# Performance work log

Measured on AMD Instinct MI355X. Metric: run time of the kernel, lower is better.

## Reference

```python
import jax, jax.numpy as jnp
import numpy as np

HEIGHT = 32
SIGMA = 2.0
NUM_NEGATIVE = 4096
N, C = 32, 512
L = HEIGHT * HEIGHT


def _grid_weight(height: int, sigma: float) -> jnp.ndarray:
    # distance_weights: pairwise Euclidean distance between grid points
    ii, jj = np.meshgrid(np.arange(height), np.arange(height), indexing='ij')
    coords = np.stack([ii.ravel(), jj.ravel()], axis=1).astype(np.float32)  # [L, 2]
    d2 = ((coords[:, None, :] - coords[None, :, :]) ** 2).sum(-1)  # squared dist [L, L]
    w = -(0.5 / sigma ** 2) * d2
    np.fill_diagonal(w, -np.inf)
    return jax.nn.softmax(jnp.asarray(w, dtype=jnp.float32), axis=1)


def setup_inputs() -> dict:
    key = jax.random.key(0)
    k1, k2 = jax.random.split(key)
    embedding = jax.random.normal(k1, (N, L, C), dtype=jnp.float32)
    weight = _grid_weight(HEIGHT, SIGMA)  # [L, L] softmax-normalized grid kernel
    neg_indices = jax.random.randint(k2, (NUM_NEGATIVE,), 0, N * L, dtype=jnp.int64)
    return {"embedding": embedding, "weight": weight, "neg_indices": neg_indices}


def reference(embedding, weight, neg_indices):
    n, l, c = embedding.shape
    # F.normalize(dim=-1), eps=1e-12
    norm = jnp.maximum(jnp.linalg.norm(embedding, axis=-1, keepdims=True), 1e-12)
    e = embedding / norm  # [N, L, C]
    # target = weight @ e  (broadcast over batch)
    target = jnp.einsum('kl,nlc->nkc', weight, e)  # [N, L, C]
    sim_pos = jnp.sum(e * target, axis=-1)  # [N, L]
    flat = e.reshape(-1, c)  # [N*L, C]
    negatives = flat[neg_indices]  # [M, C]
    sim_neg = jnp.einsum('nlc,mc->nlm', e, negatives)  # [N, L, M]
    logits = jnp.concatenate([sim_pos[..., None], sim_neg], axis=2).reshape(n * l, 1 + neg_indices.shape[0])
    # CrossEntropyLoss with target class 0, mean reduction
    loss = -jnp.mean(jax.nn.log_softmax(logits, axis=-1)[:, 0])
    return loss
```

## Files before the change

kernel.cpp:

```cpp
#include <hip/hip_runtime.h>
#include <hip/hip_bf16.h>
#include <stdint.h>

#define L_DIM 1024
#define C_DIM 512
#define CB4 256
#define N_BATCH 32
#define M_NEG 4096
#define NROWS (N_BATCH * L_DIM)

typedef float f32x4 __attribute__((ext_vector_type(4)));
typedef int i32x4 __attribute__((ext_vector_type(4)));
typedef int i32x8 __attribute__((ext_vector_type(8)));

#define E4_SCALE 32.0f
#define MX_SCALE 122
#define FMT_FP4 4

template <int GOFF>
__device__ __forceinline__ void gl_lds16(const uint8_t* g, uint8_t* l) {
  __builtin_amdgcn_global_load_lds(
      (const __attribute__((address_space(1))) void*)g,
      (__attribute__((address_space(3))) void*)l, 16, GOFF, 0);
}

__device__ __forceinline__ uint32_t fp4_enc(float x) {
  const uint32_t s = (__float_as_uint(x) >> 31) << 3;
  const float a = fabsf(x);
  uint32_t c;
  c = a < 0.25f ? 0u
    : a < 0.75f ? 1u
    : a < 1.25f ? 2u
    : a < 1.75f ? 3u
    : a < 2.5f  ? 4u
    : a < 3.5f  ? 5u
    : a < 5.0f  ? 6u : 7u;
  return s | c;
}

__device__ __forceinline__ i32x8 fp4_op(i32x4 d) {
  return __builtin_shufflevector(d, d, 0, 1, 2, 3, -1, -1, -1, -1);
}

__device__ __forceinline__ int swz(int row) { return (row >> 1) & 3; }

#define WAITK(n) asm volatile("s_waitcnt vmcnt(" #n ")\n\ts_barrier" ::: "memory")

__global__ __launch_bounds__(256) void k_normalize(const float* __restrict__ emb,
                                                   uint8_t* __restrict__ out,
                                                   float* __restrict__ zerobuf,
                                                   float* __restrict__ loss_out) {
  if (blockIdx.x < 256) zerobuf[blockIdx.x * 256 + threadIdx.x] = 0.0f;
  if (blockIdx.x == 0 && threadIdx.x == 0) loss_out[0] = 0.0f;
  const int lane = threadIdx.x & 63;
  const int wave = threadIdx.x >> 6;
  const long row = (long)blockIdx.x * 4 + wave;
  const float4* src = (const float4*)(emb + row * C_DIM);
  float4 v0 = src[2 * lane];
  float4 v1 = src[2 * lane + 1];
  float ss = v0.x * v0.x + v0.y * v0.y + v0.z * v0.z + v0.w * v0.w +
             v1.x * v1.x + v1.y * v1.y + v1.z * v1.z + v1.w * v1.w;
#pragma unroll
  for (int off = 1; off < 64; off <<= 1) ss += __shfl_xor(ss, off, 64);
  const float s = E4_SCALE / fmaxf(sqrtf(ss), 1e-12f);
  uint32_t pk = fp4_enc(v0.x * s)        | (fp4_enc(v0.y * s) << 4) |
                (fp4_enc(v0.z * s) << 8) | (fp4_enc(v0.w * s) << 12) |
                (fp4_enc(v1.x * s) << 16)| (fp4_enc(v1.y * s) << 20) |
                (fp4_enc(v1.z * s) << 24)| (fp4_enc(v1.w * s) << 28);
  ((uint32_t*)(out + row * CB4))[lane] = pk;
}

__global__ __launch_bounds__(256, 2) void k_gemm_fused(
    const uint8_t* __restrict__ E4, const int* __restrict__ idx,
    const float* __restrict__ W, float* __restrict__ rowsum,
    float* __restrict__ simpos) {
  __shared__ __align__(16) unsigned char smem_raw[65536];
  uint8_t* sA = (uint8_t*)smem_raw;
  uint8_t* sB = sA + 32768;

  const int tid = threadIdx.x;
  const int lane = tid & 63;
  const int wave = tid >> 6;
  const int wm = wave >> 1, wn = wave & 1;
  const int q = lane >> 4, c16 = lane & 15;

  const int bid = blockIdx.x;
  const bool is0 = bid >= 2048;
  long rowBase, colBase, n = 0;
  if (is0) {
    const int t = bid - 2048;
    const int xcd = t & 7, slot = t >> 3;
    rowBase = (long)(xcd * 32 + (slot & 31)) * 128;
    colBase = (long)(slot >> 5) * 128;
  } else {
    const int xcd = bid & 7, slot = bid >> 3;
    n = xcd * 4 + (slot & 3);
    const int inner = slot >> 2;
    rowBase = (long)(inner & 7) * 128;
    colBase = (long)(inner >> 3) * 128;
  }
  const long aBase = is0 ? rowBase : n * L_DIM + rowBase;

  const uint8_t* pA[2];
  const uint8_t* pB[2];
#pragma unroll
  for (int r = 0; r < 2; ++r) {
    const int c = r * 256 + tid;
    const int rw = c >> 2, cb = c & 3;
    pA[r] = E4 + (aBase + rw) * CB4 + (cb ^ swz(rw)) * 16;
    const long bRow = is0 ? (long)idx[colBase + rw] : n * L_DIM + colBase + rw;
    pB[r] = E4 + bRow * CB4 + (cb ^ swz(rw)) * 16;
  }

  int ldsB[4], ldsA[4];
#pragma unroll
  for (int j = 0; j < 4; ++j) {
    const int rowB = wn * 64 + j * 16 + c16;
    ldsB[j] = rowB * 64 + (q ^ swz(rowB)) * 16;
    const int rowA = wm * 64 + j * 16 + c16;
    ldsA[j] = rowA * 64 + (q ^ swz(rowA)) * 16;
  }

  f32x4 acc[4][4] = {};

  gl_lds16<0>(pA[0], sA + tid * 16);
  gl_lds16<0>(pA[1], sA + (256 + tid) * 16);
  gl_lds16<0>(pB[0], sB + tid * 16);
  gl_lds16<0>(pB[1], sB + (256 + tid) * 16);
  gl_lds16<64>(pA[0], sA + 8192 + tid * 16);
  gl_lds16<64>(pA[1], sA + 8192 + (256 + tid) * 16);
  gl_lds16<64>(pB[0], sB + 8192 + tid * 16);
  gl_lds16<64>(pB[1], sB + 8192 + (256 + tid) * 16);
  gl_lds16<128>(pA[0], sA + 16384 + tid * 16);
  gl_lds16<128>(pA[1], sA + 16384 + (256 + tid) * 16);
  gl_lds16<128>(pB[0], sB + 16384 + tid * 16);
  gl_lds16<128>(pB[1], sB + 16384 + (256 + tid) * 16);
  gl_lds16<192>(pA[0], sA + 24576 + tid * 16);
  gl_lds16<192>(pA[1], sA + 24576 + (256 + tid) * 16);
  gl_lds16<192>(pB[0], sB + 24576 + tid * 16);
  gl_lds16<192>(pB[1], sB + 24576 + (256 + tid) * 16);

  auto kcompute = [&](int kofs) {
    i32x8 bfr[4];
#pragma unroll
    for (int j = 0; j < 4; ++j)
      bfr[j] = fp4_op(*(const i32x4*)(sB + kofs + ldsB[j]));
#pragma unroll
    for (int i = 0; i < 4; ++i) {
      i32x8 af = fp4_op(*(const i32x4*)(sA + kofs + ldsA[i]));
#pragma unroll
      for (int j = 0; j < 4; ++j)
        acc[i][j] = __builtin_amdgcn_mfma_scale_f32_16x16x128_f8f6f4(
            af, bfr[j], acc[i][j], FMT_FP4, FMT_FP4,
            0, MX_SCALE, 0, MX_SCALE);
    }
  };

  WAITK(12);
  kcompute(0);
  WAITK(8);
  kcompute(8192);
  WAITK(4);
  kcompute(16384);
  WAITK(0);
  kcompute(24576);
  __syncthreads();

  if (is0) {
    float* S = (float*)smem_raw;
#pragma unroll
    for (int i = 0; i < 4; ++i)
#pragma unroll
      for (int r = 0; r < 4; ++r) {
        const float s = __expf(acc[i][0][r]) + __expf(acc[i][1][r]) +
                        __expf(acc[i][2][r]) + __expf(acc[i][3][r]);
        S[wave * 1280 + (i * 16 + q * 4 + r) * 20 + c16] = s;
      }
    __syncthreads();
    if (tid < 128) {
      const int wm2 = tid >> 6, row64 = tid & 63;
      const float* p0 = (const float*)S + (wm2 * 2 + 0) * 1280 + row64 * 20;
      const float* p1 = (const float*)S + (wm2 * 2 + 1) * 1280 + row64 * 20;
      float4 t0 = ((const float4*)p0)[0], t1 = ((const float4*)p0)[1];
      float4 t2 = ((const float4*)p0)[2], t3 = ((const float4*)p0)[3];
      float4 u0 = ((const float4*)p1)[0], u1 = ((const float4*)p1)[1];
      float4 u2 = ((const float4*)p1)[2], u3 = ((const float4*)p1)[3];
      float v = t0.x + t0.y + t0.z + t0.w + t1.x + t1.y + t1.z + t1.w +
                t2.x + t2.y + t2.z + t2.w + t3.x + t3.y + t3.z + t3.w +
                u0.x + u0.y + u0.z + u0.w + u1.x + u1.y + u1.z + u1.w +
                u2.x + u2.y + u2.z + u2.w + u3.x + u3.y + u3.z + u3.w;
      atomicAdd(&rowsum[rowBase + tid], v);
    }
  } else {
    float* G = (float*)smem_raw;
#pragma unroll
    for (int p = 0; p < 4; ++p) {
      if (wm == (p >> 1)) {
#pragma unroll
        for (int ii = 0; ii < 2; ++ii) {
          const int i = (p & 1) * 2 + ii;
#pragma unroll
          for (int j = 0; j < 4; ++j)
#pragma unroll
            for (int r = 0; r < 4; ++r)
              G[(ii * 16 + q * 4 + r) * 132 + wn * 64 + j * 16 + c16] =
                  acc[i][j][r];
        }
      }
      __syncthreads();
      {
        const int rr = tid >> 3;
        const int chunk = tid & 7;
        const long krow = rowBase + p * 32 + rr;
        float v = 0.0f;
#pragma unroll
        for (int u = 0; u < 4; ++u) {
          const float4 g =
              *(const float4*)(G + rr * 132 + chunk * 16 + u * 4);
          const float4 w4 = *(const float4*)(W + krow * L_DIM + colBase +
                                             chunk * 16 + u * 4);
          v += g.x * w4.x + g.y * w4.y + g.z * w4.z + g.w * w4.w;
        }
        v += __shfl_xor(v, 1, 64);
        v += __shfl_xor(v, 2, 64);
        v += __shfl_xor(v, 4, 64);
        if (chunk == 0) atomicAdd(&simpos[n * L_DIM + krow], v);
      }
      __syncthreads();
    }
  }
}

__global__ __launch_bounds__(256) void k_finalize(const float* __restrict__ rowsum,
                                                  const float* __restrict__ simpos,
                                                  float* __restrict__ out) {
  const int gid = blockIdx.x * 256 + threadIdx.x;
  const float sp = simpos[gid];
  float v = __logf(rowsum[gid] + __expf(sp)) - sp;
#pragma unroll
  for (int off = 1; off < 64; off <<= 1) v += __shfl_xor(v, off, 64);
  __shared__ float ws[4];
  if ((threadIdx.x & 63) == 0) ws[threadIdx.x >> 6] = v;
  __syncthreads();
  if (threadIdx.x == 0)
    atomicAdd(out, (ws[0] + ws[1] + ws[2] + ws[3]) * (1.0f / (float)NROWS));
}

extern "C" void kernel_launch(void* const* d_in, const int* in_sizes, int n_in,
                              void* d_out, int out_size, void* d_ws, size_t ws_size,
                              hipStream_t stream) {
  const float* emb = (const float*)d_in[0];
  const float* weight = (const float*)d_in[1];
  const int* negidx = (const int*)d_in[2];
  float* out = (float*)d_out;
  char* ws = (char*)d_ws;

  uint8_t* E4 = (uint8_t*)ws;
  float* rowsum = (float*)(ws + 8388608);
  float* simpos = (float*)(ws + 8519680);

  k_normalize<<<NROWS / 4, 256, 0, stream>>>(emb, E4, rowsum, out);
  k_gemm_fused<<<10240, 256, 0, stream>>>(E4, negidx, weight, rowsum, simpos);
  k_finalize<<<NROWS / 256, 256, 0, stream>>>(rowsum, simpos, out);
}
```

Before: 180.8 us.

## Halve LDS with double-buffered K stages and do epilogue reductions in registers

Shared memory per block drops from 64KB to 32KB by reusing two K-stage buffers. The last two stages are issued only after the earlier ones have been consumed, with a barrier guarding each reuse. Launch bounds are raised to allow 4 blocks per CU. The epilogues no longer stage results through LDS: row sums and the weighted positive similarity are reduced with lane shuffles and written by atomics directly from registers. This trades full upfront prefetch for higher occupancy and fewer block-wide syncs, but issues more atomics (one per wave-row instead of per block-row) and uses strided uncoalesced W loads.

After: 185.2 us. 1.02x slower.

```diff
diff --git a/kernel.cpp b/kernel.cpp
--- a/kernel.cpp
+++ b/kernel.cpp
@@ -45,6 +45,7 @@
 __device__ __forceinline__ int swz(int row) { return (row >> 1) & 3; }
 
 #define WAITK(n) asm volatile("s_waitcnt vmcnt(" #n ")\n\ts_barrier" ::: "memory")
+#define BARRIER() asm volatile("s_barrier" ::: "memory")
 
 __global__ __launch_bounds__(256) void k_normalize(const float* __restrict__ emb,
                                                    uint8_t* __restrict__ out,
@@ -70,13 +71,13 @@
   ((uint32_t*)(out + row * CB4))[lane] = pk;
 }
 
-__global__ __launch_bounds__(256, 2) void k_gemm_fused(
+__global__ __launch_bounds__(256, 4) void k_gemm_fused(
     const uint8_t* __restrict__ E4, const int* __restrict__ idx,
     const float* __restrict__ W, float* __restrict__ rowsum,
     float* __restrict__ simpos) {
-  __shared__ __align__(16) unsigned char smem_raw[65536];
+  __shared__ __align__(16) unsigned char smem_raw[32768];
   uint8_t* sA = (uint8_t*)smem_raw;
-  uint8_t* sB = sA + 32768;
+  uint8_t* sB = sA + 16384;
 
   const int tid = threadIdx.x;
   const int lane = tid & 63;
@@ -123,6 +124,22 @@
 
   f32x4 acc[4][4] = {};
 
+  auto kcompute = [&](int kofs) {
+    i32x8 bfr[4];
+#pragma unroll
+    for (int j = 0; j < 4; ++j)
+      bfr[j] = fp4_op(*(const i32x4*)(sB + kofs + ldsB[j]));
+#pragma unroll
+    for (int i = 0; i < 4; ++i) {
+      i32x8 af = fp4_op(*(const i32x4*)(sA + kofs + ldsA[i]));
+#pragma unroll
+      for (int j = 0; j < 4; ++j)
+        acc[i][j] = __builtin_amdgcn_mfma_scale_f32_16x16x128_f8f6f4(
+            af, bfr[j], acc[i][j], FMT_FP4, FMT_FP4,
+            0, MX_SCALE, 0, MX_SCALE);
+    }
+  };
+
   gl_lds16<0>(pA[0], sA + tid * 16);
   gl_lds16<0>(pA[1], sA + (256 + tid) * 16);
   gl_lds16<0>(pB[0], sB + tid * 16);
@@ -131,103 +148,57 @@
   gl_lds16<64>(pA[1], sA + 8192 + (256 + tid) * 16);
   gl_lds16<64>(pB[0], sB + 8192 + tid * 16);
   gl_lds16<64>(pB[1], sB + 8192 + (256 + tid) * 16);
-  gl_lds16<128>(pA[0], sA + 16384 + tid * 16);
-  gl_lds16<128>(pA[1], sA + 16384 + (256 + tid) * 16);
-  gl_lds16<128>(pB[0], sB + 16384 + tid * 16);
-  gl_lds16<128>(pB[1], sB + 16384 + (256 + tid) * 16);
-  gl_lds16<192>(pA[0], sA + 24576 + tid * 16);
-  gl_lds16<192>(pA[1], sA + 24576 + (256 + tid) * 16);
-  gl_lds16<192>(pB[0], sB + 24576 + tid * 16);
-  gl_lds16<192>(pB[1], sB + 24576 + (256 + tid) * 16);
-
-  auto kcompute = [&](int kofs) {
-    i32x8 bfr[4];
-#pragma unroll
-    for (int j = 0; j < 4; ++j)
-      bfr[j] = fp4_op(*(const i32x4*)(sB + kofs + ldsB[j]));
-#pragma unroll
-    for (int i = 0; i < 4; ++i) {
-      i32x8 af = fp4_op(*(const i32x4*)(sA + kofs + ldsA[i]));
-#pragma unroll
-      for (int j = 0; j < 4; ++j)
-        acc[i][j] = __builtin_amdgcn_mfma_scale_f32_16x16x128_f8f6f4(
-            af, bfr[j], acc[i][j], FMT_FP4, FMT_FP4,
-            0, MX_SCALE, 0, MX_SCALE);
-    }
-  };
-
-  WAITK(12);
+
+  WAITK(4);
   kcompute(0);
-  WAITK(8);
+  BARRIER();
+  gl_lds16<128>(pA[0], sA + tid * 16);
+  gl_lds16<128>(pA[1], sA + (256 + tid) * 16);
+  gl_lds16<128>(pB[0], sB + tid * 16);
+  gl_lds16<128>(pB[1], sB + (256 + tid) * 16);
+  WAITK(4);
   kcompute(8192);
+  BARRIER();
+  gl_lds16<192>(pA[0], sA + 8192 + tid * 16);
+  gl_lds16<192>(pA[1], sA + 8192 + (256 + tid) * 16);
+  gl_lds16<192>(pB[0], sB + 8192 + tid * 16);
+  gl_lds16<192>(pB[1], sB + 8192 + (256 + tid) * 16);
   WAITK(4);
-  kcompute(16384);
+  kcompute(0);
   WAITK(0);
-  kcompute(24576);
-  __syncthreads();
+  kcompute(8192);
 
   if (is0) {
-    float* S = (float*)smem_raw;
 #pragma unroll
     for (int i = 0; i < 4; ++i)
 #pragma unroll
       for (int r = 0; r < 4; ++r) {
-        const float s = __expf(acc[i][0][r]) + __expf(acc[i][1][r]) +
-                        __expf(acc[i][2][r]) + __expf(acc[i][3][r]);
-        S[wave * 1280 + (i * 16 + q * 4 + r) * 20 + c16] = s;
+        float s = __expf(acc[i][0][r]) + __expf(acc[i][1][r]) +
+                  __expf(acc[i][2][r]) + __expf(acc[i][3][r]);
+        s += __shfl_xor(s, 1, 64);
+        s += __shfl_xor(s, 2, 64);
+        s += __shfl_xor(s, 4, 64);
+        s += __shfl_xor(s, 8, 64);
+        if (c16 == 0)
+          atomicAdd(&rowsum[rowBase + wm * 64 + i * 16 + q * 4 + r], s);
       }
-    __syncthreads();
-    if (tid < 128) {
-      const int wm2 = tid >> 6, row64 = tid & 63;
-      const float* p0 = (const float*)S + (wm2 * 2 + 0) * 1280 + row64 * 20;
-      const float* p1 = (const float*)S + (wm2 * 2 + 1) * 1280 + row64 * 20;
-      float4 t0 = ((const float4*)p0)[0], t1 = ((const float4*)p0)[1];
-      float4 t2 = ((const float4*)p0)[2], t3 = ((const float4*)p0)[3];
-      float4 u0 = ((const float4*)p1)[0], u1 = ((const float4*)p1)[1];
-      float4 u2 = ((const float4*)p1)[2], u3 = ((const float4*)p1)[3];
-      float v = t0.x + t0.y + t0.z + t0.w + t1.x + t1.y + t1.z + t1.w +
-                t2.x + t2.y + t2.z + t2.w + t3.x + t3.y + t3.z + t3.w +
-                u0.x + u0.y + u0.z + u0.w + u1.x + u1.y + u1.z + u1.w +
-                u2.x + u2.y + u2.z + u2.w + u3.x + u3.y + u3.z + u3.w;
-      atomicAdd(&rowsum[rowBase + tid], v);
-    }
   } else {
-    float* G = (float*)smem_raw;
-#pragma unroll
-    for (int p = 0; p < 4; ++p) {
-      if (wm == (p >> 1)) {
-#pragma unroll
-        for (int ii = 0; ii < 2; ++ii) {
-          const int i = (p & 1) * 2 + ii;
-#pragma unroll
-          for (int j = 0; j < 4; ++j)
-#pragma unroll
-            for (int r = 0; r < 4; ++r)
-              G[(ii * 16 + q * 4 + r) * 132 + wn * 64 + j * 16 + c16] =
-                  acc[i][j][r];
-        }
-      }
-      __syncthreads();
-      {
-        const int rr = tid >> 3;
-        const int chunk = tid & 7;
-        const long krow = rowBase + p * 32 + rr;
-        float v = 0.0f;
-#pragma unroll
-        for (int u = 0; u < 4; ++u) {
-          const float4 g =
-              *(const float4*)(G + rr * 132 + chunk * 16 + u * 4);
-          const float4 w4 = *(const float4*)(W + krow * L_DIM + colBase +
-                                             chunk * 16 + u * 4);
-          v += g.x * w4.x + g.y * w4.y + g.z * w4.z + g.w * w4.w;
-        }
+    const float* Wp = W + (rowBase + wm * 64) * L_DIM + colBase + wn * 64 + c16;
+#pragma unroll
+    for (int i = 0; i < 4; ++i)
+#pragma unroll
+      for (int r = 0; r < 4; ++r) {
+        const float* wrow = Wp + (i * 16 + q * 4 + r) * L_DIM;
+        float v = acc[i][0][r] * wrow[0]  + acc[i][1][r] * wrow[16] +
+                  acc[i][2][r] * wrow[32] + acc[i][3][r] * wrow[48];
         v += __shfl_xor(v, 1, 64);
         v += __shfl_xor(v, 2, 64);
         v += __shfl_xor(v, 4, 64);
-        if (chunk == 0) atomicAdd(&simpos[n * L_DIM + krow], v);
+        v += __shfl_xor(v, 8, 64);
+        if (c16 == 0)
+          atomicAdd(&simpos[n * L_DIM + rowBase + wm * 64 + i * 16 + q * 4 + r],
+                    v);
       }
-      __syncthreads();
-    }
   }
 }
 
```
